# Optimization experiments

Measured on AMD Instinct MI355X. Metric: run time of the kernel, lower is better.

The kernel has to match this reference:

```python
import jax, jax.numpy as jnp
import numpy as np

N, E, F, H, G = 50000, 640000, 128, 128, 64


def setup_inputs() -> dict:
    key = jax.random.key(0)
    ks = jax.random.split(key, 10)
    x = jax.random.normal(ks[0], (N, F), dtype=jnp.float32)
    edge_index = jax.random.randint(ks[1], (2, E), 0, N)
    batch = jnp.sort(jax.random.randint(ks[2], (N,), 0, G))

    def glorot(k, shp):
        return jax.random.normal(k, shp, dtype=jnp.float32) * np.float32(1.0 / np.sqrt(shp[0]))

    W1 = glorot(ks[3], (F, H)); b1 = jnp.zeros((H,), jnp.float32)
    W2 = glorot(ks[4], (H, H)); b2 = jnp.zeros((H,), jnp.float32)
    W3 = glorot(ks[5], (H, H)); b3 = jnp.zeros((H,), jnp.float32)
    W4 = glorot(ks[6], (H, 2)); b4 = jnp.zeros((2,), jnp.float32)
    return {"x": x, "W1": W1, "b1": b1, "W2": W2, "b2": b2,
            "W3": W3, "b3": b3, "W4": W4, "b4": b4,
            "edge_index": edge_index, "batch": batch, "num_graphs": G}


def reference(x, W1, b1, W2, b2, W3, b3, W4, b4, edge_index, batch, num_graphs):
    n = x.shape[0]
    loop = jnp.arange(n, dtype=edge_index.dtype)
    src = jnp.concatenate([edge_index[0], loop])  # with self-loops (PyG GCNConv default)
    dst = jnp.concatenate([edge_index[1], loop])
    # symmetric degree normalization: D^{-1/2} (A+I) D^{-1/2}
    deg = jax.ops.segment_sum(jnp.ones_like(src, dtype=x.dtype), dst, num_segments=n)
    dinv = jnp.where(deg > 0, jax.lax.rsqrt(deg), 0.0)
    norm = (dinv[src] * dinv[dst])[:, None]  # [E+N, 1]

    def gcn_conv(h, W, b):
        m = h @ W                                   # transform first (F->H), then propagate
        agg = jax.ops.segment_sum(m[src] * norm, dst, num_segments=n)
        return agg + b

    h = jax.nn.relu(gcn_conv(x, W1, b1))
    h = jax.nn.relu(gcn_conv(h, W2, b2))
    g = jax.ops.segment_max(h, batch, num_segments=num_graphs)  # global_max_pool
    z = jax.nn.relu(g @ W3 + b3)                    # dropout is identity in eval
    logits = z @ W4 + b4
    return jax.nn.log_softmax(logits, axis=1)
```

## Files before the change

kernel.cpp:

```cpp
#include <hip/hip_runtime.h>
#include <hip/hip_bf16.h>
#include <math.h>

#define HDIM 128
#define SCAN_B 256
#define NBLK 256

typedef short bfrag __attribute__((ext_vector_type(8)));
typedef float f32x4 __attribute__((ext_vector_type(4)));

__device__ inline unsigned short f2bf_rne(float x) {
    unsigned u = __float_as_uint(x);
    u = (u + 0x7fffu + ((u >> 16) & 1u)) >> 16;
    return (unsigned short)u;
}
__device__ inline float bf_lo(unsigned u) { return __uint_as_float(u << 16); }
__device__ inline float bf_hi(unsigned u) { return __uint_as_float(u & 0xffff0000u); }


__device__ inline void hist_body(int b, const int* __restrict__ dst,
                                 int* __restrict__ hist, int E, int chunk, int nbuck) {
    __shared__ int hl[256];
    int t = threadIdx.x;
    hl[t] = 0;
    __syncthreads();
    int start = b * chunk, end = min(E, start + chunk);
    for (int e = start + t; e < end; e += 256) atomicAdd(&hl[dst[e] >> 8], 1);
    __syncthreads();
    if (t < nbuck) hist[t * NBLK + b] = hl[t];
}

__device__ inline void wfrag_body(int b, const float* __restrict__ W1,
                                  const float* __restrict__ W2,
                                  unsigned short* __restrict__ w1h,
                                  unsigned short* __restrict__ w1l,
                                  unsigned short* __restrict__ w2h,
                                  unsigned short* __restrict__ w2l) {
    const float* W = (b < 64) ? W1 : W2;
    unsigned short* whi = (b < 64) ? w1h : w2h;
    unsigned short* wlo = (b < 64) ? w1l : w2l;
    int idx = (b & 63) * 256 + threadIdx.x;
    int k = idx >> 7;
    int n = idx & 127;
    int kt = k >> 5, q = (k >> 3) & 3, j = k & 7;
    int lm = n >> 3, nt = n & 7;
    int lane = q * 16 + lm;
    int o = ((kt * 8 + nt) * 64 + lane) * 8 + j;
    float x = W[idx];
    unsigned short hb = f2bf_rne(x);
    float hf = __uint_as_float(((unsigned)hb) << 16);
    unsigned short lb = f2bf_rne(x - hf);
    whi[o] = hb;
    wlo[o] = lb;
}

__device__ inline void scatter_body(int b, const int* __restrict__ srcv,
                                    const int* __restrict__ dstv,
                                    const int* __restrict__ hscan,
                                    int2* __restrict__ sorted,
                                    int E, int chunk, int nbuck) {
    __shared__ int cur[256];
    int t = threadIdx.x;
    if (t < nbuck) cur[t] = hscan[t * NBLK + b];
    __syncthreads();
    int start = b * chunk, end = min(E, start + chunk);
    for (int e = start + t; e < end; e += 256) {
        int d = dstv[e];
        int pos = atomicAdd(&cur[d >> 8], 1);
        sorted[pos] = make_int2(srcv[e], d);
    }
}

#define GBM 64
__device__ inline void gemm_f32_body(int b, const float* __restrict__ A,
                                     const unsigned short* __restrict__ whi,
                                     const unsigned short* __restrict__ wlo,
                                     unsigned short* __restrict__ C, int Nrows) {
    int tid = threadIdx.x;
    int w = tid >> 6, L = tid & 63;
    int lm = L & 15, lq = L >> 4;
    int row0 = b * GBM + w * 16;

    f32x4 acc[8];
#pragma unroll
    for (int nt = 0; nt < 8; ++nt) acc[nt] = (f32x4)(0.f);

#pragma unroll
    for (int kt = 0; kt < 4; ++kt) {
        int gr = row0 + lm;
        float4 v0 = make_float4(0.f, 0.f, 0.f, 0.f);
        float4 v1 = v0;
        if (gr < Nrows) {
            const float* p = &A[(size_t)gr * HDIM + kt * 32 + lq * 8];
            v0 = *(const float4*)p;
            v1 = *(const float4*)(p + 4);
        }
        float xv[8] = {v0.x, v0.y, v0.z, v0.w, v1.x, v1.y, v1.z, v1.w};
        bfrag ah, al;
#pragma unroll
        for (int j = 0; j < 8; ++j) {
            float x = xv[j];
            unsigned short hb = f2bf_rne(x);
            float hf = __uint_as_float(((unsigned)hb) << 16);
            unsigned short lb = f2bf_rne(x - hf);
            ah[j] = (short)hb;
            al[j] = (short)lb;
        }
#pragma unroll
        for (int nt = 0; nt < 8; ++nt) {
            int o = ((kt * 8 + nt) * 64 + L) * 8;
            bfrag wh = *(const bfrag*)&whi[o];
            bfrag wl = *(const bfrag*)&wlo[o];
            acc[nt] = __builtin_amdgcn_mfma_f32_16x16x32_bf16(ah, wh, acc[nt], 0, 0, 0);
            acc[nt] = __builtin_amdgcn_mfma_f32_16x16x32_bf16(al, wh, acc[nt], 0, 0, 0);
            acc[nt] = __builtin_amdgcn_mfma_f32_16x16x32_bf16(ah, wl, acc[nt], 0, 0, 0);
        }
    }

#pragma unroll
    for (int i = 0; i < 4; ++i) {
        int gr = row0 + lq * 4 + i;
        if (gr < Nrows) {
            bfrag e;
#pragma unroll
            for (int nt = 0; nt < 8; ++nt) e[nt] = (short)f2bf_rne(acc[nt][i]);
            *(bfrag*)&C[(size_t)gr * HDIM + lm * 8] = e;
        }
    }
}

__global__ __launch_bounds__(256) void mega1_kernel(const int* __restrict__ dst,
                                                    int* __restrict__ hist, int E,
                                                    int chunk, int nbuck,
                                                    const float* __restrict__ W1,
                                                    const float* __restrict__ W2,
                                                    unsigned short* __restrict__ w1h,
                                                    unsigned short* __restrict__ w1l,
                                                    unsigned short* __restrict__ w2h,
                                                    unsigned short* __restrict__ w2l) {
    int b = blockIdx.x;
    if (b < NBLK) hist_body(b, dst, hist, E, chunk, nbuck);
    else wfrag_body(b - NBLK, W1, W2, w1h, w1l, w2h, w2l);
}

__global__ __launch_bounds__(256) void mega3_kernel(const int* __restrict__ srcv,
                                                    const int* __restrict__ dstv,
                                                    const int* __restrict__ hscan,
                                                    int2* __restrict__ sorted,
                                                    int E, int chunk, int nbuck,
                                                    const float* __restrict__ A,
                                                    const unsigned short* __restrict__ whi,
                                                    const unsigned short* __restrict__ wlo,
                                                    unsigned short* __restrict__ C, int Nrows) {
    int b = blockIdx.x;
    if (b < NBLK) scatter_body(b, srcv, dstv, hscan, sorted, E, chunk, nbuck);
    else gemm_f32_body(b - NBLK, A, whi, wlo, C, Nrows);
}

__global__ __launch_bounds__(SCAN_B) void scan1_kernel(const int* __restrict__ in,
                                                       int* __restrict__ out,
                                                       int* __restrict__ sums, int n) {
    __shared__ int s[SCAN_B];
    int t = threadIdx.x;
    int idx = blockIdx.x * SCAN_B + t;
    int v = (idx < n) ? in[idx] : 0;
    s[t] = v;
    __syncthreads();
    for (int off = 1; off < SCAN_B; off <<= 1) {
        int x = (t >= off) ? s[t - off] : 0;
        __syncthreads();
        s[t] += x;
        __syncthreads();
    }
    if (idx < n) out[idx] = s[t];
    if (t == SCAN_B - 1) sums[blockIdx.x] = s[t];
}

__global__ __launch_bounds__(SCAN_B) void scan3_kernel(const int* __restrict__ in,
                                                       int* __restrict__ inout,
                                                       const int* __restrict__ sums,
                                                       int n) {
    __shared__ int s[SCAN_B];
    int t = threadIdx.x;
    int b = blockIdx.x;
    s[t] = (t < b) ? sums[t] : 0;
    __syncthreads();
    for (int off = SCAN_B / 2; off > 0; off >>= 1) {
        if (t < off) s[t] += s[t + off];
        __syncthreads();
    }
    int base = s[0];
    int idx = b * SCAN_B + t;
    if (idx < n) inout[idx] = inout[idx] - in[idx] + base;
}

__global__ __launch_bounds__(256) void csr_kernel(const int2* __restrict__ sorted,
                                                  const int* __restrict__ hscan,
                                                  int* __restrict__ rowstart,
                                                  float* __restrict__ dinv,
                                                  int* __restrict__ csr,
                                                  int N, int E, int nbuck) {
    __shared__ int cnt[256];
    __shared__ int s[256];
    __shared__ int cur[256];
    int b = blockIdx.x;
    int t = threadIdx.x;
    int start = hscan[b * NBLK];
    int end = (b + 1 < nbuck) ? hscan[(b + 1) * NBLK] : E;
    cnt[t] = 0;
    __syncthreads();
    for (int e = start + t; e < end; e += 256)
        atomicAdd(&cnt[sorted[e].y & 255], 1);
    __syncthreads();
    int v = cnt[t];
    s[t] = v;
    __syncthreads();
    for (int off = 1; off < 256; off <<= 1) {
        int x = (t >= off) ? s[t - off] : 0;
        __syncthreads();
        s[t] += x;
        __syncthreads();
    }
    int excl = s[t] - v;
    int node = b * 256 + t;
    if (node < N) {
        rowstart[node] = start + excl;
        dinv[node] = rsqrtf((float)(v + 1));
    }
    if (b == nbuck - 1 && t == 0) rowstart[N] = E;
    cur[t] = start + excl;
    __syncthreads();
    for (int e = start + t; e < end; e += 256) {
        int2 ed = sorted[e];
        int pos = atomicAdd(&cur[ed.y & 255], 1);
        csr[pos] = ed.x;
    }
}

template <bool W>
__device__ inline void qacc(float* acc, uint4 uv, float wt) {
    if (W) {
        acc[0] = fmaf(wt, bf_lo(uv.x), acc[0]);
        acc[1] = fmaf(wt, bf_hi(uv.x), acc[1]);
        acc[2] = fmaf(wt, bf_lo(uv.y), acc[2]);
        acc[3] = fmaf(wt, bf_hi(uv.y), acc[3]);
        acc[4] = fmaf(wt, bf_lo(uv.z), acc[4]);
        acc[5] = fmaf(wt, bf_hi(uv.z), acc[5]);
        acc[6] = fmaf(wt, bf_lo(uv.w), acc[6]);
        acc[7] = fmaf(wt, bf_hi(uv.w), acc[7]);
    } else {
        acc[0] += bf_lo(uv.x); acc[1] += bf_hi(uv.x);
        acc[2] += bf_lo(uv.y); acc[3] += bf_hi(uv.y);
        acc[4] += bf_lo(uv.z); acc[5] += bf_hi(uv.z);
        acc[6] += bf_lo(uv.w); acc[7] += bf_hi(uv.w);
    }
}

template <bool W>
__device__ inline void qgather(const uint4* __restrict__ m4,
                               const int* __restrict__ csr,
                               const float* __restrict__ dinv,
                               int p, int pend, int t, float* acc) {
    for (; p + 8 <= pend; p += 8) {
        int s0 = csr[p], s1 = csr[p + 1], s2 = csr[p + 2], s3 = csr[p + 3];
        int s4 = csr[p + 4], s5 = csr[p + 5], s6 = csr[p + 6], s7 = csr[p + 7];
        float w0 = 0.f, w1 = 0.f, w2 = 0.f, w3 = 0.f;
        float w4 = 0.f, w5 = 0.f, w6 = 0.f, w7 = 0.f;
        if (W) {
            w0 = dinv[s0]; w1 = dinv[s1]; w2 = dinv[s2]; w3 = dinv[s3];
            w4 = dinv[s4]; w5 = dinv[s5]; w6 = dinv[s6]; w7 = dinv[s7];
        }
        uint4 u0 = m4[(size_t)s0 * 16 + t];
        uint4 u1 = m4[(size_t)s1 * 16 + t];
        uint4 u2 = m4[(size_t)s2 * 16 + t];
        uint4 u3 = m4[(size_t)s3 * 16 + t];
        uint4 u4 = m4[(size_t)s4 * 16 + t];
        uint4 u5 = m4[(size_t)s5 * 16 + t];
        uint4 u6 = m4[(size_t)s6 * 16 + t];
        uint4 u7 = m4[(size_t)s7 * 16 + t];
        qacc<W>(acc, u0, w0); qacc<W>(acc, u1, w1);
        qacc<W>(acc, u2, w2); qacc<W>(acc, u3, w3);
        qacc<W>(acc, u4, w4); qacc<W>(acc, u5, w5);
        qacc<W>(acc, u6, w6); qacc<W>(acc, u7, w7);
    }
    if (p + 4 <= pend) {
        int s0 = csr[p], s1 = csr[p + 1], s2 = csr[p + 2], s3 = csr[p + 3];
        float w0 = 0.f, w1 = 0.f, w2 = 0.f, w3 = 0.f;
        if (W) { w0 = dinv[s0]; w1 = dinv[s1]; w2 = dinv[s2]; w3 = dinv[s3]; }
        uint4 u0 = m4[(size_t)s0 * 16 + t];
        uint4 u1 = m4[(size_t)s1 * 16 + t];
        uint4 u2 = m4[(size_t)s2 * 16 + t];
        uint4 u3 = m4[(size_t)s3 * 16 + t];
        qacc<W>(acc, u0, w0); qacc<W>(acc, u1, w1);
        qacc<W>(acc, u2, w2); qacc<W>(acc, u3, w3);
        p += 4;
    }
    if (p + 2 <= pend) {
        int s0 = csr[p], s1 = csr[p + 1];
        float w0 = 0.f, w1 = 0.f;
        if (W) { w0 = dinv[s0]; w1 = dinv[s1]; }
        uint4 u0 = m4[(size_t)s0 * 16 + t];
        uint4 u1 = m4[(size_t)s1 * 16 + t];
        qacc<W>(acc, u0, w0); qacc<W>(acc, u1, w1);
        p += 2;
    }
    if (p < pend) {
        int s0 = csr[p];
        float w0 = W ? dinv[s0] : 0.f;
        uint4 u0 = m4[(size_t)s0 * 16 + t];
        qacc<W>(acc, u0, w0);
    }
}

__device__ inline int degree_perm(const int* __restrict__ rowstart,
                                  int* lens, int* perm, int n) {
    if (threadIdx.x < 16) {
        int nn = blockIdx.x * 16 + threadIdx.x;
        lens[threadIdx.x] = (nn < n) ? (rowstart[nn + 1] - rowstart[nn]) : -1;
    }
    __syncthreads();
    if (threadIdx.x < 16) {
        int L = lens[threadIdx.x];
        int r = 0;
#pragma unroll
        for (int j = 0; j < 16; ++j) {
            int Lj = lens[j];
            r += (Lj > L || (Lj == L && j < (int)threadIdx.x)) ? 1 : 0;
        }
        perm[r] = threadIdx.x;
    }
    __syncthreads();
    return perm[threadIdx.x >> 4];
}

__global__ __launch_bounds__(256) void agg_gemm_kernel(
        const uint4* __restrict__ m4,
        const int* __restrict__ rowstart,
        const int* __restrict__ csr,
        const float* __restrict__ dinv,
        const float* __restrict__ bias,
        const unsigned short* __restrict__ whi,
        const unsigned short* __restrict__ wlo,
        uint4* __restrict__ out_m, int n) {
    __shared__ unsigned short hbuf[16][HDIM + 8];
    __shared__ float cbuf[16][HDIM + 4];
    __shared__ int lens[16];
    __shared__ int perm[16];
    int t = threadIdx.x & 15;

    int pnl = degree_perm(rowstart, lens, perm, n);
    int node = blockIdx.x * 16 + pnl;

    unsigned short hv[8] = {0, 0, 0, 0, 0, 0, 0, 0};
    if (node < n) {
        float dd = dinv[node];
        float acc[8];
        uint4 u = m4[(size_t)node * 16 + t];
        acc[0] = dd * bf_lo(u.x); acc[1] = dd * bf_hi(u.x);
        acc[2] = dd * bf_lo(u.y); acc[3] = dd * bf_hi(u.y);
        acc[4] = dd * bf_lo(u.z); acc[5] = dd * bf_hi(u.z);
        acc[6] = dd * bf_lo(u.w); acc[7] = dd * bf_hi(u.w);
        qgather<true>(m4, csr, dinv, rowstart[node], rowstart[node + 1], t, acc);
        float4 b0 = *(const float4*)&bias[t * 8];
        float4 b1 = *(const float4*)&bias[t * 8 + 4];
        float bb[8] = {b0.x, b0.y, b0.z, b0.w, b1.x, b1.y, b1.z, b1.w};
#pragma unroll
        for (int j = 0; j < 8; ++j)
            hv[j] = f2bf_rne(fmaxf(fmaf(dd, acc[j], bb[j]), 0.f));
    }
    *(uint4*)&hbuf[pnl][t * 8] = *(uint4*)hv;
    __syncthreads();

    int w = threadIdx.x >> 6, L = threadIdx.x & 63;
    int lm = L & 15, lq = L >> 4;
    f32x4 acc2[2];
    acc2[0] = (f32x4)(0.f);
    acc2[1] = (f32x4)(0.f);
#pragma unroll
    for (int kt = 0; kt < 4; ++kt) {
        bfrag a = *(const bfrag*)&hbuf[lm][kt * 32 + lq * 8];
#pragma unroll
        for (int q2 = 0; q2 < 2; ++q2) {
            int nt = w * 2 + q2;
            int o = ((kt * 8 + nt) * 64 + L) * 8;
            bfrag wh = *(const bfrag*)&whi[o];
            bfrag wl = *(const bfrag*)&wlo[o];
            acc2[q2] = __builtin_amdgcn_mfma_f32_16x16x32_bf16(a, wh, acc2[q2], 0, 0, 0);
            acc2[q2] = __builtin_amdgcn_mfma_f32_16x16x32_bf16(a, wl, acc2[q2], 0, 0, 0);
        }
    }
#pragma unroll
    for (int q2 = 0; q2 < 2; ++q2) {
        int nt = w * 2 + q2;
#pragma unroll
        for (int i = 0; i < 4; ++i) cbuf[lq * 4 + i][lm * 8 + nt] = acc2[q2][i];
    }
    __syncthreads();

    int nl = threadIdx.x >> 4;
    int node_e = blockIdx.x * 16 + nl;
    if (node_e < n) {
        float dde = dinv[node_e];
        float4 r0 = *(const float4*)&cbuf[nl][t * 8];
        float4 r1 = *(const float4*)&cbuf[nl][t * 8 + 4];
        unsigned short ev[8];
        ev[0] = f2bf_rne(dde * r0.x); ev[1] = f2bf_rne(dde * r0.y);
        ev[2] = f2bf_rne(dde * r0.z); ev[3] = f2bf_rne(dde * r0.w);
        ev[4] = f2bf_rne(dde * r1.x); ev[5] = f2bf_rne(dde * r1.y);
        ev[6] = f2bf_rne(dde * r1.z); ev[7] = f2bf_rne(dde * r1.w);
        out_m[(size_t)node_e * 16 + t] = *(uint4*)ev;
    }
}

__global__ __launch_bounds__(256) void agg_pool_kernel(const uint4* __restrict__ m4,
                                                       const int* __restrict__ rowstart,
                                                       const int* __restrict__ csr,
                                                       const float* __restrict__ dinv,
                                                       const float* __restrict__ bias,
                                                       const int* __restrict__ batch,
                                                       unsigned int* __restrict__ g, int n) {
    __shared__ float smx[16][HDIM];
    __shared__ int sgid[16];
    __shared__ int lens[16];
    __shared__ int perm[16];
    int t = threadIdx.x & 15;

    int pnl = degree_perm(rowstart, lens, perm, n);
    int node = blockIdx.x * 16 + pnl;
    bool valid = node < n;
    if (valid) {
        float dd = dinv[node];
        float acc[8];
        uint4 u = m4[(size_t)node * 16 + t];
        acc[0] = bf_lo(u.x); acc[1] = bf_hi(u.x);
        acc[2] = bf_lo(u.y); acc[3] = bf_hi(u.y);
        acc[4] = bf_lo(u.z); acc[5] = bf_hi(u.z);
        acc[6] = bf_lo(u.w); acc[7] = bf_hi(u.w);
        qgather<false>(m4, csr, dinv, rowstart[node], rowstart[node + 1], t, acc);
        float4 b0 = *(const float4*)&bias[t * 8];
        float4 b1 = *(const float4*)&bias[t * 8 + 4];
        float4 r0, r1;
        r0.x = fmaxf(fmaf(dd, acc[0], b0.x), 0.f);
        r0.y = fmaxf(fmaf(dd, acc[1], b0.y), 0.f);
        r0.z = fmaxf(fmaf(dd, acc[2], b0.z), 0.f);
        r0.w = fmaxf(fmaf(dd, acc[3], b0.w), 0.f);
        r1.x = fmaxf(fmaf(dd, acc[4], b1.x), 0.f);
        r1.y = fmaxf(fmaf(dd, acc[5], b1.y), 0.f);
        r1.z = fmaxf(fmaf(dd, acc[6], b1.z), 0.f);
        r1.w = fmaxf(fmaf(dd, acc[7], b1.w), 0.f);
        *(float4*)&smx[pnl][t * 8] = r0;
        *(float4*)&smx[pnl][t * 8 + 4] = r1;
    }
    if (t == 0) sgid[pnl] = valid ? batch[node] : -1;
    __syncthreads();
    if (threadIdx.x < HDIM) {
        int c = threadIdx.x;
        int curg = -1;
        float run = 0.f;
#pragma unroll
        for (int r = 0; r < 16; ++r) {
            int gg = sgid[r];
            if (gg < 0) continue;
            if (gg != curg) {
                if (curg >= 0) atomicMax(&g[curg * HDIM + c], __float_as_uint(run));
                curg = gg;
                run = smx[r][c];
            } else {
                run = fmaxf(run, smx[r][c]);
            }
        }
        if (curg >= 0) atomicMax(&g[curg * HDIM + c], __float_as_uint(run));
    }
}

__global__ __launch_bounds__(128) void mlp_kernel(const unsigned int* __restrict__ gbits,
                                                  const float* __restrict__ W3,
                                                  const float* __restrict__ b3,
                                                  const float* __restrict__ W4,
                                                  const float* __restrict__ b4,
                                                  float* __restrict__ out) {
    __shared__ float gs[HDIM];
    __shared__ float r0[HDIM];
    __shared__ float r1[HDIM];
    int j = threadIdx.x;
    int b = blockIdx.x;
    gs[j] = __uint_as_float(gbits[b * HDIM + j]);
    __syncthreads();
    float acc = b3[j];
#pragma unroll 8
    for (int k = 0; k < HDIM; ++k) acc = fmaf(gs[k], W3[k * HDIM + j], acc);
    float z = fmaxf(acc, 0.f);
    r0[j] = z * W4[j * 2 + 0];
    r1[j] = z * W4[j * 2 + 1];
    __syncthreads();
    for (int off = 64; off > 0; off >>= 1) {
        if (j < off) {
            r0[j] += r0[j + off];
            r1[j] += r1[j + off];
        }
        __syncthreads();
    }
    if (j == 0) {
        float l0 = r0[0] + b4[0];
        float l1 = r1[0] + b4[1];
        float mx = fmaxf(l0, l1);
        float lse = mx + logf(expf(l0 - mx) + expf(l1 - mx));
        out[b * 2 + 0] = l0 - lse;
        out[b * 2 + 1] = l1 - lse;
    }
}

extern "C" void kernel_launch(void* const* d_in, const int* in_sizes, int n_in,
                              void* d_out, int out_size, void* d_ws, size_t ws_size,
                              hipStream_t stream) {
    const float* x  = (const float*)d_in[0];
    const float* W1 = (const float*)d_in[1];
    const float* b1 = (const float*)d_in[2];
    const float* W2 = (const float*)d_in[3];
    const float* b2 = (const float*)d_in[4];
    const float* W3 = (const float*)d_in[5];
    const float* b3 = (const float*)d_in[6];
    const float* W4 = (const float*)d_in[7];
    const float* b4 = (const float*)d_in[8];
    const int* ei    = (const int*)d_in[9];
    const int* batch = (const int*)d_in[10];

    const int N = in_sizes[0] / HDIM;
    const int E = in_sizes[9] / 2;
    const int G = out_size / 2;
    const int* src = ei;
    const int* dst = ei + E;

    const int nbuck = (N + 255) >> 8;
    const int nscan = nbuck * NBLK;
    const int chunk = (E + NBLK - 1) / NBLK;

    const int Nr = ((N + 63) / 64) * 64;
    char* wsb = (char*)d_ws;
    size_t o = 0;
    unsigned int* g = (unsigned int*)(wsb + o); o += (size_t)G * HDIM * 4;
    size_t zero_bytes = o;
    int* hist = (int*)(wsb + o);           o += (size_t)nscan * 4;
    int* hscan = (int*)(wsb + o);          o += (size_t)nscan * 4;
    int* sums = (int*)(wsb + o);           o += 256 * 4;
    int* rowstart = (int*)(wsb + o);       o += (size_t)(Nr + 64) * 4;
    float* dinv = (float*)(wsb + o);       o += (size_t)Nr * 4;
    int2* sorted = (int2*)(wsb + o);       o += (size_t)E * 8;
    int* csr = (int*)(wsb + o);            o += (size_t)E * 4;
    unsigned short* wf1h = (unsigned short*)(wsb + o); o += (size_t)HDIM * HDIM * 2;
    unsigned short* wf1l = (unsigned short*)(wsb + o); o += (size_t)HDIM * HDIM * 2;
    unsigned short* wf2h = (unsigned short*)(wsb + o); o += (size_t)HDIM * HDIM * 2;
    unsigned short* wf2l = (unsigned short*)(wsb + o); o += (size_t)HDIM * HDIM * 2;
    unsigned short* m = (unsigned short*)(wsb + o);    o += (size_t)Nr * HDIM * 2;
    unsigned short* m2 = (unsigned short*)(wsb + o);   o += (size_t)Nr * HDIM * 2;
    (void)ws_size; (void)n_in;

    (void)hipMemsetAsync(d_ws, 0, zero_bytes, stream);

    int sblocks = (nscan + SCAN_B - 1) / SCAN_B;
    int gemm_blocks = (N + GBM - 1) / GBM;
    int agg_blocks = (N + 15) / 16;

    mega1_kernel<<<NBLK + 128, 256, 0, stream>>>(dst, hist, E, chunk, nbuck,
                                                 W1, W2, wf1h, wf1l, wf2h, wf2l);
    scan1_kernel<<<sblocks, SCAN_B, 0, stream>>>(hist, hscan, sums, nscan);
    scan3_kernel<<<sblocks, SCAN_B, 0, stream>>>(hist, hscan, sums, nscan);
    mega3_kernel<<<NBLK + gemm_blocks, 256, 0, stream>>>(src, dst, hscan, sorted,
                                                         E, chunk, nbuck,
                                                         x, wf1h, wf1l, m, N);
    csr_kernel<<<nbuck, 256, 0, stream>>>(sorted, hscan, rowstart, dinv, csr, N, E, nbuck);
    agg_gemm_kernel<<<agg_blocks, 256, 0, stream>>>((const uint4*)m, rowstart, csr,
                                                    dinv, b1, wf2h, wf2l,
                                                    (uint4*)m2, N);
    agg_pool_kernel<<<agg_blocks, 256, 0, stream>>>((const uint4*)m2, rowstart, csr,
                                                    dinv, b2, batch, g, N);
    mlp_kernel<<<G, 128, 0, stream>>>(g, W3, b3, W4, b4, (float*)d_out);
}
```

Measured before the change: 201.7 us.

## Pre-scale layer-1 features by dinv in CSR kernel to drop per-edge weight loads

The first-layer GEMM now writes fp32 output to a temporary buffer. The CSR build kernel then multiplies each row by its source-node dinv and converts it to bf16, so the layer-1 gather no longer loads dinv per neighbour and can use plain adds. The gather loop also loads CSR indices as int4 vectors after an alignment prologue, and caches rowstart values in shared memory. In exchange it adds an extra fp32 write and read of the full N×128 feature matrix, plus a serial conversion pass inside the CSR kernel.

```diff
diff --git a/kernel.cpp b/kernel.cpp
--- a/kernel.cpp
+++ b/kernel.cpp
@@ -75,7 +75,7 @@
 __device__ inline void gemm_f32_body(int b, const float* __restrict__ A,
                                      const unsigned short* __restrict__ whi,
                                      const unsigned short* __restrict__ wlo,
-                                     unsigned short* __restrict__ C, int Nrows) {
+                                     float* __restrict__ C, int Nrows) {
     int tid = threadIdx.x;
     int w = tid >> 6, L = tid & 63;
     int lm = L & 15, lq = L >> 4;
@@ -121,10 +121,10 @@
     for (int i = 0; i < 4; ++i) {
         int gr = row0 + lq * 4 + i;
         if (gr < Nrows) {
-            bfrag e;
-#pragma unroll
-            for (int nt = 0; nt < 8; ++nt) e[nt] = (short)f2bf_rne(acc[nt][i]);
-            *(bfrag*)&C[(size_t)gr * HDIM + lm * 8] = e;
+            float4 o0 = make_float4(acc[0][i], acc[1][i], acc[2][i], acc[3][i]);
+            float4 o1 = make_float4(acc[4][i], acc[5][i], acc[6][i], acc[7][i]);
+            *(float4*)&C[(size_t)gr * HDIM + lm * 8] = o0;
+            *(float4*)&C[(size_t)gr * HDIM + lm * 8 + 4] = o1;
         }
     }
 }
@@ -151,7 +151,7 @@
                                                     const float* __restrict__ A,
                                                     const unsigned short* __restrict__ whi,
                                                     const unsigned short* __restrict__ wlo,
-                                                    unsigned short* __restrict__ C, int Nrows) {
+                                                    float* __restrict__ C, int Nrows) {
     int b = blockIdx.x;
     if (b < NBLK) scatter_body(b, srcv, dstv, hscan, sorted, E, chunk, nbuck);
     else gemm_f32_body(b - NBLK, A, whi, wlo, C, Nrows);
@@ -199,10 +199,13 @@
                                                   int* __restrict__ rowstart,
                                                   float* __restrict__ dinv,
                                                   int* __restrict__ csr,
+                                                  const float* __restrict__ mtmp,
+                                                  unsigned short* __restrict__ m,
                                                   int N, int E, int nbuck) {
     __shared__ int cnt[256];
     __shared__ int s[256];
     __shared__ int cur[256];
+    __shared__ float sdv[256];
     int b = blockIdx.x;
     int t = threadIdx.x;
     int start = hscan[b * NBLK];
@@ -223,9 +226,11 @@
     }
     int excl = s[t] - v;
     int node = b * 256 + t;
+    float dv = rsqrtf((float)(v + 1));
+    sdv[t] = dv;
     if (node < N) {
         rowstart[node] = start + excl;
-        dinv[node] = rsqrtf((float)(v + 1));
+        dinv[node] = dv;
     }
     if (b == nbuck - 1 && t == 0) rowstart[N] = E;
     cur[t] = start + excl;
@@ -235,88 +240,76 @@
         int pos = atomicAdd(&cur[ed.y & 255], 1);
         csr[pos] = ed.x;
     }
-}
-
-template <bool W>
-__device__ inline void qacc(float* acc, uint4 uv, float wt) {
-    if (W) {
-        acc[0] = fmaf(wt, bf_lo(uv.x), acc[0]);
-        acc[1] = fmaf(wt, bf_hi(uv.x), acc[1]);
-        acc[2] = fmaf(wt, bf_lo(uv.y), acc[2]);
-        acc[3] = fmaf(wt, bf_hi(uv.y), acc[3]);
-        acc[4] = fmaf(wt, bf_lo(uv.z), acc[4]);
-        acc[5] = fmaf(wt, bf_hi(uv.z), acc[5]);
-        acc[6] = fmaf(wt, bf_lo(uv.w), acc[6]);
-        acc[7] = fmaf(wt, bf_hi(uv.w), acc[7]);
-    } else {
-        acc[0] += bf_lo(uv.x); acc[1] += bf_hi(uv.x);
-        acc[2] += bf_lo(uv.y); acc[3] += bf_hi(uv.y);
-        acc[4] += bf_lo(uv.z); acc[5] += bf_hi(uv.z);
-        acc[6] += bf_lo(uv.w); acc[7] += bf_hi(uv.w);
-    }
-}
-
-template <bool W>
+    const float4* mt4 = (const float4*)mtmp;
+    uint2* m2p = (uint2*)m;
+    for (int idx = t; idx < 256 * 32; idx += 256) {
+        int r = idx >> 5, c = idx & 31;
+        int nn = b * 256 + r;
+        if (nn < N) {
+            float4 v4 = mt4[(size_t)nn * 32 + c];
+            float dd = sdv[r];
+            unsigned short ev[4];
+            ev[0] = f2bf_rne(dd * v4.x);
+            ev[1] = f2bf_rne(dd * v4.y);
+            ev[2] = f2bf_rne(dd * v4.z);
+            ev[3] = f2bf_rne(dd * v4.w);
+            m2p[(size_t)nn * 32 + c] = *(uint2*)ev;
+        }
+    }
+}
+
+#define QACC(UV)                                       \
+    acc[0] += bf_lo((UV).x); acc[1] += bf_hi((UV).x);  \
+    acc[2] += bf_lo((UV).y); acc[3] += bf_hi((UV).y);  \
+    acc[4] += bf_lo((UV).z); acc[5] += bf_hi((UV).z);  \
+    acc[6] += bf_lo((UV).w); acc[7] += bf_hi((UV).w);
+
 __device__ inline void qgather(const uint4* __restrict__ m4,
                                const int* __restrict__ csr,
-                               const float* __restrict__ dinv,
                                int p, int pend, int t, float* acc) {
+    while (p < pend && (p & 3)) {
+        uint4 u0 = m4[(size_t)csr[p] * 16 + t];
+        QACC(u0);
+        ++p;
+    }
     for (; p + 8 <= pend; p += 8) {
-        int s0 = csr[p], s1 = csr[p + 1], s2 = csr[p + 2], s3 = csr[p + 3];
-        int s4 = csr[p + 4], s5 = csr[p + 5], s6 = csr[p + 6], s7 = csr[p + 7];
-        float w0 = 0.f, w1 = 0.f, w2 = 0.f, w3 = 0.f;
-        float w4 = 0.f, w5 = 0.f, w6 = 0.f, w7 = 0.f;
-        if (W) {
-            w0 = dinv[s0]; w1 = dinv[s1]; w2 = dinv[s2]; w3 = dinv[s3];
-            w4 = dinv[s4]; w5 = dinv[s5]; w6 = dinv[s6]; w7 = dinv[s7];
-        }
-        uint4 u0 = m4[(size_t)s0 * 16 + t];
-        uint4 u1 = m4[(size_t)s1 * 16 + t];
-        uint4 u2 = m4[(size_t)s2 * 16 + t];
-        uint4 u3 = m4[(size_t)s3 * 16 + t];
-        uint4 u4 = m4[(size_t)s4 * 16 + t];
-        uint4 u5 = m4[(size_t)s5 * 16 + t];
-        uint4 u6 = m4[(size_t)s6 * 16 + t];
-        uint4 u7 = m4[(size_t)s7 * 16 + t];
-        qacc<W>(acc, u0, w0); qacc<W>(acc, u1, w1);
-        qacc<W>(acc, u2, w2); qacc<W>(acc, u3, w3);
-        qacc<W>(acc, u4, w4); qacc<W>(acc, u5, w5);
-        qacc<W>(acc, u6, w6); qacc<W>(acc, u7, w7);
+        int4 i0 = *(const int4*)&csr[p];
+        int4 i1 = *(const int4*)&csr[p + 4];
+        uint4 u0 = m4[(size_t)i0.x * 16 + t];
+        uint4 u1 = m4[(size_t)i0.y * 16 + t];
+        uint4 u2 = m4[(size_t)i0.z * 16 + t];
+        uint4 u3 = m4[(size_t)i0.w * 16 + t];
+        uint4 u4 = m4[(size_t)i1.x * 16 + t];
+        uint4 u5 = m4[(size_t)i1.y * 16 + t];
+        uint4 u6 = m4[(size_t)i1.z * 16 + t];
+        uint4 u7 = m4[(size_t)i1.w * 16 + t];
+        QACC(u0); QACC(u1); QACC(u2); QACC(u3);
+        QACC(u4); QACC(u5); QACC(u6); QACC(u7);
     }
     if (p + 4 <= pend) {
-        int s0 = csr[p], s1 = csr[p + 1], s2 = csr[p + 2], s3 = csr[p + 3];
-        float w0 = 0.f, w1 = 0.f, w2 = 0.f, w3 = 0.f;
-        if (W) { w0 = dinv[s0]; w1 = dinv[s1]; w2 = dinv[s2]; w3 = dinv[s3]; }
-        uint4 u0 = m4[(size_t)s0 * 16 + t];
-        uint4 u1 = m4[(size_t)s1 * 16 + t];
-        uint4 u2 = m4[(size_t)s2 * 16 + t];
-        uint4 u3 = m4[(size_t)s3 * 16 + t];
-        qacc<W>(acc, u0, w0); qacc<W>(acc, u1, w1);
-        qacc<W>(acc, u2, w2); qacc<W>(acc, u3, w3);
+        int4 i0 = *(const int4*)&csr[p];
+        uint4 u0 = m4[(size_t)i0.x * 16 + t];
+        uint4 u1 = m4[(size_t)i0.y * 16 + t];
+        uint4 u2 = m4[(size_t)i0.z * 16 + t];
+        uint4 u3 = m4[(size_t)i0.w * 16 + t];
+        QACC(u0); QACC(u1); QACC(u2); QACC(u3);
         p += 4;
     }
-    if (p + 2 <= pend) {
-        int s0 = csr[p], s1 = csr[p + 1];
-        float w0 = 0.f, w1 = 0.f;
-        if (W) { w0 = dinv[s0]; w1 = dinv[s1]; }
-        uint4 u0 = m4[(size_t)s0 * 16 + t];
-        uint4 u1 = m4[(size_t)s1 * 16 + t];
-        qacc<W>(acc, u0, w0); qacc<W>(acc, u1, w1);
-        p += 2;
-    }
-    if (p < pend) {
-        int s0 = csr[p];
-        float w0 = W ? dinv[s0] : 0.f;
-        uint4 u0 = m4[(size_t)s0 * 16 + t];
-        qacc<W>(acc, u0, w0);
+    while (p < pend) {
+        uint4 u0 = m4[(size_t)csr[p] * 16 + t];
+        QACC(u0);
+        ++p;
     }
 }
 
 __device__ inline int degree_perm(const int* __restrict__ rowstart,
-                                  int* lens, int* perm, int n) {
+                                  int* lens, int* rs, int* perm, int n) {
     if (threadIdx.x < 16) {
         int nn = blockIdx.x * 16 + threadIdx.x;
-        lens[threadIdx.x] = (nn < n) ? (rowstart[nn + 1] - rowstart[nn]) : -1;
+        int a = (nn < n) ? rowstart[nn] : 0;
+        int bnd = (nn < n) ? rowstart[nn + 1] : 0;
+        rs[threadIdx.x] = a;
+        lens[threadIdx.x] = (nn < n) ? (bnd - a) : -1;
     }
     __syncthreads();
     if (threadIdx.x < 16) {
@@ -345,10 +338,11 @@
     __shared__ unsigned short hbuf[16][HDIM + 8];
     __shared__ float cbuf[16][HDIM + 4];
     __shared__ int lens[16];
+    __shared__ int rs[16];
     __shared__ int perm[16];
     int t = threadIdx.x & 15;
 
-    int pnl = degree_perm(rowstart, lens, perm, n);
+    int pnl = degree_perm(rowstart, lens, rs, perm, n);
     int node = blockIdx.x * 16 + pnl;
 
     unsigned short hv[8] = {0, 0, 0, 0, 0, 0, 0, 0};
@@ -356,11 +350,12 @@
         float dd = dinv[node];
         float acc[8];
         uint4 u = m4[(size_t)node * 16 + t];
-        acc[0] = dd * bf_lo(u.x); acc[1] = dd * bf_hi(u.x);
-        acc[2] = dd * bf_lo(u.y); acc[3] = dd * bf_hi(u.y);
-        acc[4] = dd * bf_lo(u.z); acc[5] = dd * bf_hi(u.z);
-        acc[6] = dd * bf_lo(u.w); acc[7] = dd * bf_hi(u.w);
-        qgather<true>(m4, csr, dinv, rowstart[node], rowstart[node + 1], t, acc);
+        acc[0] = bf_lo(u.x); acc[1] = bf_hi(u.x);
+        acc[2] = bf_lo(u.y); acc[3] = bf_hi(u.y);
+        acc[4] = bf_lo(u.z); acc[5] = bf_hi(u.z);
+        acc[6] = bf_lo(u.w); acc[7] = bf_hi(u.w);
+        int p0 = rs[pnl];
+        qgather(m4, csr, p0, p0 + lens[pnl], t, acc);
         float4 b0 = *(const float4*)&bias[t * 8];
         float4 b1 = *(const float4*)&bias[t * 8 + 4];
         float bb[8] = {b0.x, b0.y, b0.z, b0.w, b1.x, b1.y, b1.z, b1.w};
@@ -422,10 +417,11 @@
     __shared__ float smx[16][HDIM];
     __shared__ int sgid[16];
     __shared__ int lens[16];
+    __shared__ int rs[16];
     __shared__ int perm[16];
     int t = threadIdx.x & 15;
 
-    int pnl = degree_perm(rowstart, lens, perm, n);
+    int pnl = degree_perm(rowstart, lens, rs, perm, n);
     int node = blockIdx.x * 16 + pnl;
     bool valid = node < n;
     if (valid) {
@@ -436,7 +432,8 @@
         acc[2] = bf_lo(u.y); acc[3] = bf_hi(u.y);
         acc[4] = bf_lo(u.z); acc[5] = bf_hi(u.z);
         acc[6] = bf_lo(u.w); acc[7] = bf_hi(u.w);
-        qgather<false>(m4, csr, dinv, rowstart[node], rowstart[node + 1], t, acc);
+        int p0 = rs[pnl];
+        qgather(m4, csr, p0, p0 + lens[pnl], t, acc);
         float4 b0 = *(const float4*)&bias[t * 8];
         float4 b1 = *(const float4*)&bias[t * 8 + 4];
         float4 r0, r1;
@@ -553,6 +550,7 @@
     unsigned short* wf2l = (unsigned short*)(wsb + o); o += (size_t)HDIM * HDIM * 2;
     unsigned short* m = (unsigned short*)(wsb + o);    o += (size_t)Nr * HDIM * 2;
     unsigned short* m2 = (unsigned short*)(wsb + o);   o += (size_t)Nr * HDIM * 2;
+    float* mtmp = (float*)(wsb + o);       o += (size_t)Nr * HDIM * 4;
     (void)ws_size; (void)n_in;
 
     (void)hipMemsetAsync(d_ws, 0, zero_bytes, stream);
@@ -567,8 +565,9 @@
     scan3_kernel<<<sblocks, SCAN_B, 0, stream>>>(hist, hscan, sums, nscan);
     mega3_kernel<<<NBLK + gemm_blocks, 256, 0, stream>>>(src, dst, hscan, sorted,
                                                          E, chunk, nbuck,
-                                                         x, wf1h, wf1l, m, N);
-    csr_kernel<<<nbuck, 256, 0, stream>>>(sorted, hscan, rowstart, dinv, csr, N, E, nbuck);
+                                                         x, wf1h, wf1l, mtmp, N);
+    csr_kernel<<<nbuck, 256, 0, stream>>>(sorted, hscan, rowstart, dinv, csr,
+                                          mtmp, m, N, E, nbuck);
     agg_gemm_kernel<<<agg_blocks, 256, 0, stream>>>((const uint4*)m, rowstart, csr,
                                                     dinv, b1, wf2h, wf2l,
                                                     (uint4*)m2, N);
```

Measured after the change: 216.4 us. +7.3%, slower.

## Process two nodes per 16-thread group with interleaved dual-row gather

Applied to the files above, without the earlier changes.

The aggregation kernels now handle 32 nodes per block, with each 16-lane group gathering two degree-paired rows at once through an interleaved dual_gather loop. The two-row MFMA tile covers 32 rows, and the max-pool reduction scans 32 rows per block. The goal is more independent loads in flight per thread and half as many blocks, with the weight fragments reused across two row tiles. The cost is higher register pressure and shared memory per block, and fewer blocks may leave parts of the GPU underused.

```diff
diff --git a/kernel.cpp b/kernel.cpp
--- a/kernel.cpp
+++ b/kernel.cpp
@@ -238,7 +238,7 @@
 }
 
 template <bool W>
-__device__ inline void qacc(float* acc, uint4 uv, float wt) {
+__device__ inline void qacc1(float* acc, uint4 uv, float wt) {
     if (W) {
         acc[0] = fmaf(wt, bf_lo(uv.x), acc[0]);
         acc[1] = fmaf(wt, bf_hi(uv.x), acc[1]);
@@ -278,10 +278,10 @@
         uint4 u5 = m4[(size_t)s5 * 16 + t];
         uint4 u6 = m4[(size_t)s6 * 16 + t];
         uint4 u7 = m4[(size_t)s7 * 16 + t];
-        qacc<W>(acc, u0, w0); qacc<W>(acc, u1, w1);
-        qacc<W>(acc, u2, w2); qacc<W>(acc, u3, w3);
-        qacc<W>(acc, u4, w4); qacc<W>(acc, u5, w5);
-        qacc<W>(acc, u6, w6); qacc<W>(acc, u7, w7);
+        qacc1<W>(acc, u0, w0); qacc1<W>(acc, u1, w1);
+        qacc1<W>(acc, u2, w2); qacc1<W>(acc, u3, w3);
+        qacc1<W>(acc, u4, w4); qacc1<W>(acc, u5, w5);
+        qacc1<W>(acc, u6, w6); qacc1<W>(acc, u7, w7);
     }
     if (p + 4 <= pend) {
         int s0 = csr[p], s1 = csr[p + 1], s2 = csr[p + 2], s3 = csr[p + 3];
@@ -291,8 +291,8 @@
         uint4 u1 = m4[(size_t)s1 * 16 + t];
         uint4 u2 = m4[(size_t)s2 * 16 + t];
         uint4 u3 = m4[(size_t)s3 * 16 + t];
-        qacc<W>(acc, u0, w0); qacc<W>(acc, u1, w1);
-        qacc<W>(acc, u2, w2); qacc<W>(acc, u3, w3);
+        qacc1<W>(acc, u0, w0); qacc1<W>(acc, u1, w1);
+        qacc1<W>(acc, u2, w2); qacc1<W>(acc, u3, w3);
         p += 4;
     }
     if (p + 2 <= pend) {
@@ -301,36 +301,71 @@
         if (W) { w0 = dinv[s0]; w1 = dinv[s1]; }
         uint4 u0 = m4[(size_t)s0 * 16 + t];
         uint4 u1 = m4[(size_t)s1 * 16 + t];
-        qacc<W>(acc, u0, w0); qacc<W>(acc, u1, w1);
+        qacc1<W>(acc, u0, w0); qacc1<W>(acc, u1, w1);
         p += 2;
     }
     if (p < pend) {
         int s0 = csr[p];
         float w0 = W ? dinv[s0] : 0.f;
         uint4 u0 = m4[(size_t)s0 * 16 + t];
-        qacc<W>(acc, u0, w0);
-    }
-}
-
-__device__ inline int degree_perm(const int* __restrict__ rowstart,
-                                  int* lens, int* perm, int n) {
-    if (threadIdx.x < 16) {
-        int nn = blockIdx.x * 16 + threadIdx.x;
-        lens[threadIdx.x] = (nn < n) ? (rowstart[nn + 1] - rowstart[nn]) : -1;
-    }
-    __syncthreads();
-    if (threadIdx.x < 16) {
+        qacc1<W>(acc, u0, w0);
+    }
+}
+
+template <bool W>
+__device__ inline void dual_gather(const uint4* __restrict__ m4,
+                                   const int* __restrict__ csr,
+                                   const float* __restrict__ dinv,
+                                   int pA, int pAe, int pB, int pBe, int t,
+                                   float* aA, float* aB) {
+    while (pA + 4 <= pAe && pB + 4 <= pBe) {
+        int a0 = csr[pA], a1 = csr[pA + 1], a2 = csr[pA + 2], a3 = csr[pA + 3];
+        int b0 = csr[pB], b1 = csr[pB + 1], b2 = csr[pB + 2], b3 = csr[pB + 3];
+        float wa0 = 0.f, wa1 = 0.f, wa2 = 0.f, wa3 = 0.f;
+        float wb0 = 0.f, wb1 = 0.f, wb2 = 0.f, wb3 = 0.f;
+        if (W) {
+            wa0 = dinv[a0]; wa1 = dinv[a1]; wa2 = dinv[a2]; wa3 = dinv[a3];
+            wb0 = dinv[b0]; wb1 = dinv[b1]; wb2 = dinv[b2]; wb3 = dinv[b3];
+        }
+        uint4 uA0 = m4[(size_t)a0 * 16 + t];
+        uint4 uA1 = m4[(size_t)a1 * 16 + t];
+        uint4 uA2 = m4[(size_t)a2 * 16 + t];
+        uint4 uA3 = m4[(size_t)a3 * 16 + t];
+        uint4 uB0 = m4[(size_t)b0 * 16 + t];
+        uint4 uB1 = m4[(size_t)b1 * 16 + t];
+        uint4 uB2 = m4[(size_t)b2 * 16 + t];
+        uint4 uB3 = m4[(size_t)b3 * 16 + t];
+        qacc1<W>(aA, uA0, wa0); qacc1<W>(aB, uB0, wb0);
+        qacc1<W>(aA, uA1, wa1); qacc1<W>(aB, uB1, wb1);
+        qacc1<W>(aA, uA2, wa2); qacc1<W>(aB, uB2, wb2);
+        qacc1<W>(aA, uA3, wa3); qacc1<W>(aB, uB3, wb3);
+        pA += 4; pB += 4;
+    }
+    qgather<W>(m4, csr, dinv, pA, pAe, t, aA);
+    qgather<W>(m4, csr, dinv, pB, pBe, t, aB);
+}
+
+__device__ inline void degree_perm32(const int* __restrict__ rowstart,
+                                     int* lens, int* rs, int* perm, int n) {
+    if (threadIdx.x < 32) {
+        int nn = blockIdx.x * 32 + threadIdx.x;
+        int a = (nn < n) ? rowstart[nn] : 0;
+        int b2 = (nn < n) ? rowstart[nn + 1] : 0;
+        rs[threadIdx.x] = a;
+        lens[threadIdx.x] = (nn < n) ? (b2 - a) : -1;
+    }
+    __syncthreads();
+    if (threadIdx.x < 32) {
         int L = lens[threadIdx.x];
         int r = 0;
 #pragma unroll
-        for (int j = 0; j < 16; ++j) {
+        for (int j = 0; j < 32; ++j) {
             int Lj = lens[j];
             r += (Lj > L || (Lj == L && j < (int)threadIdx.x)) ? 1 : 0;
         }
         perm[r] = threadIdx.x;
     }
     __syncthreads();
-    return perm[threadIdx.x >> 4];
 }
 
 __global__ __launch_bounds__(256) void agg_gemm_kernel(
@@ -342,73 +377,106 @@
         const unsigned short* __restrict__ whi,
         const unsigned short* __restrict__ wlo,
         uint4* __restrict__ out_m, int n) {
-    __shared__ unsigned short hbuf[16][HDIM + 8];
-    __shared__ float cbuf[16][HDIM + 4];
-    __shared__ int lens[16];
-    __shared__ int perm[16];
+    __shared__ unsigned short hbuf[32][HDIM + 8];
+    __shared__ float cbuf[32][HDIM + 4];
+    __shared__ int lens[32];
+    __shared__ int rs[32];
+    __shared__ int perm[32];
     int t = threadIdx.x & 15;
-
-    int pnl = degree_perm(rowstart, lens, perm, n);
-    int node = blockIdx.x * 16 + pnl;
-
-    unsigned short hv[8] = {0, 0, 0, 0, 0, 0, 0, 0};
-    if (node < n) {
-        float dd = dinv[node];
-        float acc[8];
-        uint4 u = m4[(size_t)node * 16 + t];
-        acc[0] = dd * bf_lo(u.x); acc[1] = dd * bf_hi(u.x);
-        acc[2] = dd * bf_lo(u.y); acc[3] = dd * bf_hi(u.y);
-        acc[4] = dd * bf_lo(u.z); acc[5] = dd * bf_hi(u.z);
-        acc[6] = dd * bf_lo(u.w); acc[7] = dd * bf_hi(u.w);
-        qgather<true>(m4, csr, dinv, rowstart[node], rowstart[node + 1], t, acc);
+    int qid = threadIdx.x >> 4;
+
+    degree_perm32(rowstart, lens, rs, perm, n);
+    int pnlA = perm[2 * qid], pnlB = perm[2 * qid + 1];
+    int nodeA = blockIdx.x * 32 + pnlA;
+    int nodeB = blockIdx.x * 32 + pnlB;
+    bool vA = nodeA < n, vB = nodeB < n;
+
+    float aA[8] = {0, 0, 0, 0, 0, 0, 0, 0};
+    float aB[8] = {0, 0, 0, 0, 0, 0, 0, 0};
+    float ddA = 0.f, ddB = 0.f;
+    if (vA) {
+        ddA = dinv[nodeA];
+        uint4 u = m4[(size_t)nodeA * 16 + t];
+        aA[0] = ddA * bf_lo(u.x); aA[1] = ddA * bf_hi(u.x);
+        aA[2] = ddA * bf_lo(u.y); aA[3] = ddA * bf_hi(u.y);
+        aA[4] = ddA * bf_lo(u.z); aA[5] = ddA * bf_hi(u.z);
+        aA[6] = ddA * bf_lo(u.w); aA[7] = ddA * bf_hi(u.w);
+    }
+    if (vB) {
+        ddB = dinv[nodeB];
+        uint4 u = m4[(size_t)nodeB * 16 + t];
+        aB[0] = ddB * bf_lo(u.x); aB[1] = ddB * bf_hi(u.x);
+        aB[2] = ddB * bf_lo(u.y); aB[3] = ddB * bf_hi(u.y);
+        aB[4] = ddB * bf_lo(u.z); aB[5] = ddB * bf_hi(u.z);
+        aB[6] = ddB * bf_lo(u.w); aB[7] = ddB * bf_hi(u.w);
+    }
+    {
+        int pA = rs[pnlA], lA = lens[pnlA];
+        int pB = rs[pnlB], lB = lens[pnlB];
+        dual_gather<true>(m4, csr, dinv, pA, pA + max(lA, 0),
+                          pB, pB + max(lB, 0), t, aA, aB);
+    }
+    {
         float4 b0 = *(const float4*)&bias[t * 8];
         float4 b1 = *(const float4*)&bias[t * 8 + 4];
         float bb[8] = {b0.x, b0.y, b0.z, b0.w, b1.x, b1.y, b1.z, b1.w};
-#pragma unroll
-        for (int j = 0; j < 8; ++j)
-            hv[j] = f2bf_rne(fmaxf(fmaf(dd, acc[j], bb[j]), 0.f));
-    }
-    *(uint4*)&hbuf[pnl][t * 8] = *(uint4*)hv;
+        unsigned short hvA[8], hvB[8];
+#pragma unroll
+        for (int j = 0; j < 8; ++j) {
+            hvA[j] = vA ? f2bf_rne(fmaxf(fmaf(ddA, aA[j], bb[j]), 0.f)) : (unsigned short)0;
+            hvB[j] = vB ? f2bf_rne(fmaxf(fmaf(ddB, aB[j], bb[j]), 0.f)) : (unsigned short)0;
+        }
+        *(uint4*)&hbuf[pnlA][t * 8] = *(uint4*)hvA;
+        *(uint4*)&hbuf[pnlB][t * 8] = *(uint4*)hvB;
+    }
     __syncthreads();
 
     int w = threadIdx.x >> 6, L = threadIdx.x & 63;
     int lm = L & 15, lq = L >> 4;
-    f32x4 acc2[2];
-    acc2[0] = (f32x4)(0.f);
-    acc2[1] = (f32x4)(0.f);
-#pragma unroll
-    for (int kt = 0; kt < 4; ++kt) {
-        bfrag a = *(const bfrag*)&hbuf[lm][kt * 32 + lq * 8];
+#pragma unroll
+    for (int rt = 0; rt < 2; ++rt) {
+        f32x4 acc2[2];
+        acc2[0] = (f32x4)(0.f);
+        acc2[1] = (f32x4)(0.f);
+#pragma unroll
+        for (int kt = 0; kt < 4; ++kt) {
+            bfrag a = *(const bfrag*)&hbuf[rt * 16 + lm][kt * 32 + lq * 8];
+#pragma unroll
+            for (int q2 = 0; q2 < 2; ++q2) {
+                int nt = w * 2 + q2;
+                int o = ((kt * 8 + nt) * 64 + L) * 8;
+                bfrag wh = *(const bfrag*)&whi[o];
+                bfrag wl = *(const bfrag*)&wlo[o];
+                acc2[q2] = __builtin_amdgcn_mfma_f32_16x16x32_bf16(a, wh, acc2[q2], 0, 0, 0);
+                acc2[q2] = __builtin_amdgcn_mfma_f32_16x16x32_bf16(a, wl, acc2[q2], 0, 0, 0);
+            }
+        }
 #pragma unroll
         for (int q2 = 0; q2 < 2; ++q2) {
             int nt = w * 2 + q2;
-            int o = ((kt * 8 + nt) * 64 + L) * 8;
-            bfrag wh = *(const bfrag*)&whi[o];
-            bfrag wl = *(const bfrag*)&wlo[o];
-            acc2[q2] = __builtin_amdgcn_mfma_f32_16x16x32_bf16(a, wh, acc2[q2], 0, 0, 0);
-            acc2[q2] = __builtin_amdgcn_mfma_f32_16x16x32_bf16(a, wl, acc2[q2], 0, 0, 0);
-        }
-    }
-#pragma unroll
-    for (int q2 = 0; q2 < 2; ++q2) {
-        int nt = w * 2 + q2;
-#pragma unroll
-        for (int i = 0; i < 4; ++i) cbuf[lq * 4 + i][lm * 8 + nt] = acc2[q2][i];
+#pragma unroll
+            for (int i = 0; i < 4; ++i)
+                cbuf[rt * 16 + lq * 4 + i][lm * 8 + nt] = acc2[q2][i];
+        }
     }
     __syncthreads();
 
     int nl = threadIdx.x >> 4;
-    int node_e = blockIdx.x * 16 + nl;
-    if (node_e < n) {
-        float dde = dinv[node_e];
-        float4 r0 = *(const float4*)&cbuf[nl][t * 8];
-        float4 r1 = *(const float4*)&cbuf[nl][t * 8 + 4];
-        unsigned short ev[8];
-        ev[0] = f2bf_rne(dde * r0.x); ev[1] = f2bf_rne(dde * r0.y);
-        ev[2] = f2bf_rne(dde * r0.z); ev[3] = f2bf_rne(dde * r0.w);
-        ev[4] = f2bf_rne(dde * r1.x); ev[5] = f2bf_rne(dde * r1.y);
-        ev[6] = f2bf_rne(dde * r1.z); ev[7] = f2bf_rne(dde * r1.w);
-        out_m[(size_t)node_e * 16 + t] = *(uint4*)ev;
+#pragma unroll
+    for (int half = 0; half < 2; ++half) {
+        int r = half * 16 + nl;
+        int node_e = blockIdx.x * 32 + r;
+        if (node_e < n) {
+            float dde = dinv[node_e];
+            float4 r0 = *(const float4*)&cbuf[r][t * 8];
+            float4 r1 = *(const float4*)&cbuf[r][t * 8 + 4];
+            unsigned short ev[8];
+            ev[0] = f2bf_rne(dde * r0.x); ev[1] = f2bf_rne(dde * r0.y);
+            ev[2] = f2bf_rne(dde * r0.z); ev[3] = f2bf_rne(dde * r0.w);
+            ev[4] = f2bf_rne(dde * r1.x); ev[5] = f2bf_rne(dde * r1.y);
+            ev[6] = f2bf_rne(dde * r1.z); ev[7] = f2bf_rne(dde * r1.w);
+            out_m[(size_t)node_e * 16 + t] = *(uint4*)ev;
+        }
     }
 }
 
@@ -419,46 +487,87 @@
                                                        const float* __restrict__ bias,
                                                        const int* __restrict__ batch,
                                                        unsigned int* __restrict__ g, int n) {
-    __shared__ float smx[16][HDIM];
-    __shared__ int sgid[16];
-    __shared__ int lens[16];
-    __shared__ int perm[16];
+    __shared__ float smx[32][HDIM];
+    __shared__ int sgid[32];
+    __shared__ int lens[32];
+    __shared__ int rs[32];
+    __shared__ int perm[32];
     int t = threadIdx.x & 15;
-
-    int pnl = degree_perm(rowstart, lens, perm, n);
-    int node = blockIdx.x * 16 + pnl;
-    bool valid = node < n;
-    if (valid) {
-        float dd = dinv[node];
-        float acc[8];
-        uint4 u = m4[(size_t)node * 16 + t];
-        acc[0] = bf_lo(u.x); acc[1] = bf_hi(u.x);
-        acc[2] = bf_lo(u.y); acc[3] = bf_hi(u.y);
-        acc[4] = bf_lo(u.z); acc[5] = bf_hi(u.z);
-        acc[6] = bf_lo(u.w); acc[7] = bf_hi(u.w);
-        qgather<false>(m4, csr, dinv, rowstart[node], rowstart[node + 1], t, acc);
+    int qid = threadIdx.x >> 4;
+
+    degree_perm32(rowstart, lens, rs, perm, n);
+    int pnlA = perm[2 * qid], pnlB = perm[2 * qid + 1];
+    int nodeA = blockIdx.x * 32 + pnlA;
+    int nodeB = blockIdx.x * 32 + pnlB;
+    bool vA = nodeA < n, vB = nodeB < n;
+
+    float aA[8] = {0, 0, 0, 0, 0, 0, 0, 0};
+    float aB[8] = {0, 0, 0, 0, 0, 0, 0, 0};
+    float ddA = 0.f, ddB = 0.f;
+    if (vA) {
+        ddA = dinv[nodeA];
+        uint4 u = m4[(size_t)nodeA * 16 + t];
+        aA[0] = bf_lo(u.x); aA[1] = bf_hi(u.x);
+        aA[2] = bf_lo(u.y); aA[3] = bf_hi(u.y);
+        aA[4] = bf_lo(u.z); aA[5] = bf_hi(u.z);
+        aA[6] = bf_lo(u.w); aA[7] = bf_hi(u.w);
+    }
+    if (vB) {
+        ddB = dinv[nodeB];
+        uint4 u = m4[(size_t)nodeB * 16 + t];
+        aB[0] = bf_lo(u.x); aB[1] = bf_hi(u.x);
+        aB[2] = bf_lo(u.y); aB[3] = bf_hi(u.y);
+        aB[4] = bf_lo(u.z); aB[5] = bf_hi(u.z);
+        aB[6] = bf_lo(u.w); aB[7] = bf_hi(u.w);
+    }
+    {
+        int pA = rs[pnlA], lA = lens[pnlA];
+        int pB = rs[pnlB], lB = lens[pnlB];
+        dual_gather<false>(m4, csr, dinv, pA, pA + max(lA, 0),
+                           pB, pB + max(lB, 0), t, aA, aB);
+    }
+    {
         float4 b0 = *(const float4*)&bias[t * 8];
         float4 b1 = *(const float4*)&bias[t * 8 + 4];
-        float4 r0, r1;
-        r0.x = fmaxf(fmaf(dd, acc[0], b0.x), 0.f);
-        r0.y = fmaxf(fmaf(dd, acc[1], b0.y), 0.f);
-        r0.z = fmaxf(fmaf(dd, acc[2], b0.z), 0.f);
-        r0.w = fmaxf(fmaf(dd, acc[3], b0.w), 0.f);
-        r1.x = fmaxf(fmaf(dd, acc[4], b1.x), 0.f);
-        r1.y = fmaxf(fmaf(dd, acc[5], b1.y), 0.f);
-        r1.z = fmaxf(fmaf(dd, acc[6], b1.z), 0.f);
-        r1.w = fmaxf(fmaf(dd, acc[7], b1.w), 0.f);
-        *(float4*)&smx[pnl][t * 8] = r0;
-        *(float4*)&smx[pnl][t * 8 + 4] = r1;
-    }
-    if (t == 0) sgid[pnl] = valid ? batch[node] : -1;
+        float bb[8] = {b0.x, b0.y, b0.z, b0.w, b1.x, b1.y, b1.z, b1.w};
+        if (vA) {
+            float4 r0, r1;
+            r0.x = fmaxf(fmaf(ddA, aA[0], bb[0]), 0.f);
+            r0.y = fmaxf(fmaf(ddA, aA[1], bb[1]), 0.f);
+            r0.z = fmaxf(fmaf(ddA, aA[2], bb[2]), 0.f);
+            r0.w = fmaxf(fmaf(ddA, aA[3], bb[3]), 0.f);
+            r1.x = fmaxf(fmaf(ddA, aA[4], bb[4]), 0.f);
+            r1.y = fmaxf(fmaf(ddA, aA[5], bb[5]), 0.f);
+            r1.z = fmaxf(fmaf(ddA, aA[6], bb[6]), 0.f);
+            r1.w = fmaxf(fmaf(ddA, aA[7], bb[7]), 0.f);
+            *(float4*)&smx[pnlA][t * 8] = r0;
+            *(float4*)&smx[pnlA][t * 8 + 4] = r1;
+        }
+        if (vB) {
+            float4 r0, r1;
+            r0.x = fmaxf(fmaf(ddB, aB[0], bb[0]), 0.f);
+            r0.y = fmaxf(fmaf(ddB, aB[1], bb[1]), 0.f);
+            r0.z = fmaxf(fmaf(ddB, aB[2], bb[2]), 0.f);
+            r0.w = fmaxf(fmaf(ddB, aB[3], bb[3]), 0.f);
+            r1.x = fmaxf(fmaf(ddB, aB[4], bb[4]), 0.f);
+            r1.y = fmaxf(fmaf(ddB, aB[5], bb[5]), 0.f);
+            r1.z = fmaxf(fmaf(ddB, aB[6], bb[6]), 0.f);
+            r1.w = fmaxf(fmaf(ddB, aB[7], bb[7]), 0.f);
+            *(float4*)&smx[pnlB][t * 8] = r0;
+            *(float4*)&smx[pnlB][t * 8 + 4] = r1;
+        }
+    }
+    if (t == 0) {
+        sgid[pnlA] = vA ? batch[nodeA] : -1;
+        sgid[pnlB] = vB ? batch[nodeB] : -1;
+    }
     __syncthreads();
     if (threadIdx.x < HDIM) {
         int c = threadIdx.x;
         int curg = -1;
         float run = 0.f;
 #pragma unroll
-        for (int r = 0; r < 16; ++r) {
+        for (int r = 0; r < 32; ++r) {
             int gg = sgid[r];
             if (gg < 0) continue;
             if (gg != curg) {
@@ -559,7 +668,7 @@
 
     int sblocks = (nscan + SCAN_B - 1) / SCAN_B;
     int gemm_blocks = (N + GBM - 1) / GBM;
-    int agg_blocks = (N + 15) / 16;
+    int agg_blocks = (N + 31) / 32;
 
     mega1_kernel<<<NBLK + 128, 256, 0, stream>>>(dst, hist, E, chunk, nbuck,
                                                  W1, W2, wf1h, wf1l, wf2h, wf2l);
```

New measurement: 210.2 us. 1.04x slower.
